# Performance work log

Hardware: AMD Instinct MI355X
Metric: run time of the kernel (lower is better)

## Reference

```python
import jax, jax.numpy as jnp
import numpy as np

B, T, C, H = 16, 512, 256, 8
HS_T = C // H   # temporal head size = 32
HS_S = T // H   # spatial head size = 64
EPS = 1e-6


def _ln(x, w, b):
    m = x.mean(-1, keepdims=True)
    v = ((x - m) ** 2).mean(-1, keepdims=True)
    return (x - m) / jnp.sqrt(v + EPS) * w + b


def setup_inputs() -> dict:
    key = jax.random.key(0)
    ks = jax.random.split(key, 16)
    rn = lambda k, s, scale: jax.random.normal(k, s, dtype=jnp.float32) * scale
    inp = {
        "x_T": rn(ks[0], (B, T, C), 1.0),
        "x_S": rn(ks[1], (B, C, T), 1.0),
        # temporal attention: per-head q/k/v projections, stacked [H, hs, C]
        "Wq_t": rn(ks[2], (H, HS_T, C), C ** -0.5),
        "Wk_t": rn(ks[3], (H, HS_T, C), C ** -0.5),
        "Wv_t": rn(ks[4], (H, HS_T, C), C ** -0.5),
        "Wo": rn(ks[5], (C, C), C ** -0.5),
        # spatial attention: per-head q/k over the time axis, stacked [H, hs_s, T]
        "Wq_s": rn(ks[6], (H, HS_S, T), T ** -0.5),
        "Wk_s": rn(ks[7], (H, HS_S, T), T ** -0.5),
        # feed-forward blocks (expansion_factor=4)
        "ff1_w1": rn(ks[8], (4 * C, C), C ** -0.5),
        "ff1_b1": jnp.zeros((4 * C,), jnp.float32),
        "ff1_w2": rn(ks[9], (C, 4 * C), (4 * C) ** -0.5),
        "ff1_b2": jnp.zeros((C,), jnp.float32),
        "ff2_w1": rn(ks[10], (4 * C, C), C ** -0.5),
        "ff2_b1": jnp.zeros((4 * C,), jnp.float32),
        "ff2_w2": rn(ks[11], (C, 4 * C), (4 * C) ** -0.5),
        "ff2_b2": jnp.zeros((C,), jnp.float32),
        # layernorm affine params
        "t_ln1_w": jnp.ones((C,), jnp.float32), "t_ln1_b": jnp.zeros((C,), jnp.float32),
        "t_ln2_w": jnp.ones((C,), jnp.float32), "t_ln2_b": jnp.zeros((C,), jnp.float32),
        "s_ln1_w": jnp.ones((T,), jnp.float32), "s_ln1_b": jnp.zeros((T,), jnp.float32),
        "fus_ln_w": jnp.ones((C,), jnp.float32), "fus_ln_b": jnp.zeros((C,), jnp.float32),
    }
    return inp


def reference(x_T, x_S, Wq_t, Wk_t, Wv_t, Wo, Wq_s, Wk_s,
              ff1_w1, ff1_b1, ff1_w2, ff1_b2, ff2_w1, ff2_b1, ff2_w2, ff2_b2,
              t_ln1_w, t_ln1_b, t_ln2_w, t_ln2_b, s_ln1_w, s_ln1_b,
              fus_ln_w, fus_ln_b):
    # ---- temporal (causal) multi-head attention ----
    h = _ln(x_T, t_ln1_w, t_ln1_b)                         # [B,T,C]
    q = jnp.einsum('btc,hdc->bhtd', h, Wq_t)
    k = jnp.einsum('btc,hdc->bhtd', h, Wk_t)
    v = jnp.einsum('btc,hdc->bhtd', h, Wv_t)
    scores = jnp.einsum('bhtd,bhsd->bhts', q, k) / jnp.sqrt(jnp.float32(HS_T))
    causal = jnp.tril(jnp.ones((T, T), dtype=bool))
    scores = jnp.where(causal, scores, -jnp.inf)
    att = jax.nn.softmax(scores, axis=-1)
    o = jnp.einsum('bhts,bhsd->bhtd', att, v)              # [B,H,T,hs]
    o = o.transpose(0, 2, 1, 3).reshape(B, T, C)           # concat heads
    attn_out = o @ Wo.T
    x = x_T + attn_out
    # FFN 1
    h2 = _ln(x, t_ln2_w, t_ln2_b)
    f = jax.nn.relu(h2 @ ff1_w1.T + ff1_b1) @ ff1_w2.T + ff1_b2
    temporal_out = x + f                                   # [B,T,C]
    # ---- spatial (non-causal) attention over neurons ----
    hs = _ln(x_S, s_ln1_w, s_ln1_b)                        # [B,C,T]
    qs = jnp.einsum('bct,hdt->bhcd', hs, Wq_s)
    ks = jnp.einsum('bct,hdt->bhcd', hs, Wk_s)
    sc = jnp.einsum('bhcd,bhed->bhce', qs, ks) / jnp.sqrt(jnp.float32(HS_S))
    spatial_weights = jax.nn.softmax(sc, axis=-1).mean(axis=1)   # [B,C,C], mean over heads
    # ---- fusion ----
    fused = jnp.einsum('bce,bte->btc', spatial_weights, temporal_out)
    x2 = temporal_out + fused
    h3 = _ln(x2, fus_ln_w, fus_ln_b)
    f2 = jax.nn.relu(h3 @ ff2_w1.T + ff2_b1) @ ff2_w2.T + ff2_b2
    out = x2 + f2
    return out, spatial_weights
```

## Files before the change

### kernel.cpp

```cpp
#include <hip/hip_runtime.h>
#include <hip/hip_bf16.h>

typedef __hip_bfloat16 bf16;
typedef __attribute__((ext_vector_type(8))) short short8;
typedef __attribute__((ext_vector_type(4))) float f32x4;

#define F_BIAS 1
#define F_RELU 2
#define F_RES  4

__device__ __forceinline__ void st_out(float* p, float v){ *p = v; }
__device__ __forceinline__ void st_out(bf16* p, float v){ *p = __float2bfloat16(v); }
__device__ __forceinline__ short f2bs(float f){
  bf16 h = __float2bfloat16(f);
  return *reinterpret_cast<short*>(&h);
}

__device__ __forceinline__ void gl_lds16(const void* g, void* l){
  __builtin_amdgcn_global_load_lds(
      (const __attribute__((address_space(1))) void*)g,
      (__attribute__((address_space(3))) void*)l, 16, 0, 0);
}

__device__ __forceinline__ void lgkm_barrier(){
  asm volatile("s_waitcnt lgkmcnt(0)" ::: "memory");
  __builtin_amdgcn_s_barrier();
}

struct ProArgs {
  const float* wsrc[10];
  bf16* wdst[10];
  const float *xT, *xS, *tl1w, *tl1b, *sl1w, *sl1b;
  bf16 *hT, *hS;
};

template<int RL>
__device__ __forceinline__ void wave_ln(bf16* __restrict__ dst,
    const float* __restrict__ src, const float* __restrict__ w,
    const float* __restrict__ bvec, int row){
  int lane = threadIdx.x & 63;
  const float* s = src + (size_t)row*RL;
  float4 v0 = *(const float4*)(s + lane*4);
  float4 v1 = {0.f,0.f,0.f,0.f};
  float sum = v0.x+v0.y+v0.z+v0.w;
  float sq  = v0.x*v0.x+v0.y*v0.y+v0.z*v0.z+v0.w*v0.w;
  if (RL == 512){
    v1 = *(const float4*)(s + 256 + lane*4);
    sum += v1.x+v1.y+v1.z+v1.w;
    sq  += v1.x*v1.x+v1.y*v1.y+v1.z*v1.z+v1.w*v1.w;
  }
  #pragma unroll
  for (int off=32; off; off>>=1){
    sum += __shfl_xor(sum, off, 64);
    sq  += __shfl_xor(sq , off, 64);
  }
  const float inv = 1.0f/(float)RL;
  float mean = sum*inv;
  float rstd = rsqrtf(sq*inv - mean*mean + 1e-6f);
  float4 w0 = *(const float4*)(w + lane*4);
  float4 b0 = *(const float4*)(bvec + lane*4);
  bf16* d = dst + (size_t)row*RL;
  short4 o;
  o.x = f2bs((v0.x-mean)*rstd*w0.x + b0.x);
  o.y = f2bs((v0.y-mean)*rstd*w0.y + b0.y);
  o.z = f2bs((v0.z-mean)*rstd*w0.z + b0.z);
  o.w = f2bs((v0.w-mean)*rstd*w0.w + b0.w);
  *(short4*)((short*)d + lane*4) = o;
  if (RL == 512){
    float4 w1 = *(const float4*)(w + 256 + lane*4);
    float4 b1 = *(const float4*)(bvec + 256 + lane*4);
    short4 o1;
    o1.x = f2bs((v1.x-mean)*rstd*w1.x + b1.x);
    o1.y = f2bs((v1.y-mean)*rstd*w1.y + b1.y);
    o1.z = f2bs((v1.z-mean)*rstd*w1.z + b1.z);
    o1.w = f2bs((v1.w-mean)*rstd*w1.w + b1.w);
    *(short4*)((short*)d + 256 + lane*4) = o1;
  }
}

__global__ __launch_bounds__(256) void prologue(ProArgs a){
  int blk = blockIdx.x;
  int wid = threadIdx.x >> 6;
  if (blk < 1792){
    int v = blk*256 + threadIdx.x;
    int e = v*4;
    int seg = (e>=65536)+(e>=131072)+(e>=196608)+(e>=262144)+(e>=524288)
            + (e>=786432)+(e>=1048576)+(e>=1310720)+(e>=1572864);
    const int starts[10] = {0,65536,131072,196608,262144,524288,786432,
                            1048576,1310720,1572864};
    int off = e - starts[seg];
    float4 f = *(const float4*)(a.wsrc[seg] + off);
    short4 o;
    o.x = f2bs(f.x); o.y = f2bs(f.y); o.z = f2bs(f.z); o.w = f2bs(f.w);
    *(short4*)((short*)a.wdst[seg] + off) = o;
  } else if (blk < 1792 + 2048){
    wave_ln<256>(a.hT, a.xT, a.tl1w, a.tl1b, (blk-1792)*4 + wid);
  } else {
    wave_ln<512>(a.hS, a.xS, a.sl1w, a.sl1b, (blk-3840)*4 + wid);
  }
}

template<int BM, int BN, int BK>
__device__ __forceinline__ void gemm_body(
    short* __restrict__ AsB, short* __restrict__ BsB,
    const bf16* __restrict__ A, const bf16* __restrict__ B,
    float* __restrict__ outF, bf16* __restrict__ outB,
    const float* __restrict__ bias, const float* __restrict__ resid,
    int K, int lda, int ldb, int ldc, int flags, int m0, int n0){
  int tid = threadIdx.x;
  int w = tid>>6, lane = tid&63, quad = lane>>4, l16 = lane&15;
  constexpr int MF  = BM/32;
  constexpr int NF  = BN/32;
  constexpr int CPR = BK/8;
  constexpr int CA  = BM*CPR/256;
  constexpr int CB  = BN*CPR/256;
  int wm = (w>>1)*(BM/2), wn = (w&1)*(BN/2);
  f32x4 acc[MF][NF];
  #pragma unroll
  for (int r=0;r<MF;r++)
    #pragma unroll
    for (int j=0;j<NF;j++)
      acc[r][j] = (f32x4){0.f,0.f,0.f,0.f};

  auto stage = [&](int k0, int half){
    short* as = AsB + half*(BM*BK);
    short* bs = BsB + half*(BN*BK);
    #pragma unroll
    for (int c=0;c<CA;c++){
      int ch = tid + c*256;
      int row = ch / CPR, p = ch % CPR;
      gl_lds16(A + (size_t)(m0+row)*lda + k0 + ((p ^ (row&(CPR-1)))*8),
               &as[row*BK + p*8]);
    }
    #pragma unroll
    for (int c=0;c<CB;c++){
      int ch = tid + c*256;
      int row = ch / CPR, p = ch % CPR;
      gl_lds16(B + (size_t)(n0+row)*ldb + k0 + ((p ^ (row&(CPR-1)))*8),
               &bs[row*BK + p*8]);
    }
  };

  stage(0, 0);
  int nk = K / BK;
  for (int t = 0; t < nk; ++t){
    __syncthreads();
    if (t+1 < nk) stage((t+1)*BK, (t+1)&1);
    const short* as = AsB + (t&1)*(BM*BK);
    const short* bs = BsB + (t&1)*(BN*BK);
    #pragma unroll
    for (int ks=0; ks<BK/32; ++ks){
      short8 af[MF], bfr[NF];
      #pragma unroll
      for (int r=0;r<MF;r++){
        int rr = wm + r*16 + l16;
        af[r] = *(short8*)&as[rr*BK + (((ks*4+quad) ^ (rr&(CPR-1)))*8)];
      }
      #pragma unroll
      for (int j=0;j<NF;j++){
        int rr = wn + j*16 + l16;
        bfr[j] = *(short8*)&bs[rr*BK + (((ks*4+quad) ^ (rr&(CPR-1)))*8)];
      }
      #pragma unroll
      for (int r=0;r<MF;r++)
        #pragma unroll
        for (int j=0;j<NF;j++)
          acc[r][j] = __builtin_amdgcn_mfma_f32_16x16x32_bf16(af[r], bfr[j], acc[r][j], 0,0,0);
    }
  }
  #pragma unroll
  for (int r=0;r<MF;r++){
    int mb = m0 + wm + r*16 + quad*4;
    #pragma unroll
    for (int j=0;j<NF;j++){
      int n = n0 + wn + j*16 + l16;
      float bv = (flags & F_BIAS) ? bias[n] : 0.0f;
      #pragma unroll
      for (int e=0;e<4;e++){
        float v = acc[r][j][e] + bv;
        if (flags & F_RELU) v = fmaxf(v, 0.0f);
        long long idx = (long long)(mb+e)*ldc + n;
        if (flags & F_RES) v += resid[idx];
        if (outF) outF[idx] = v;
        if (outB) st_out(outB + idx, v);
      }
    }
  }
}

struct GArgs {
  const bf16 *A, *B;
  float* outF; bf16* outB;
  const float *bias, *resid;
  int K, lda, ldb, ldc, flags, ty;
};
__global__ __launch_bounds__(256) void gemm_dual(GArgs g0, GArgs g1, int n0){
  __shared__ __align__(16) short As[2*128*64];
  __shared__ __align__(16) short Bs[2*128*64];
  int id = blockIdx.x;
  bool first = id < n0;
  const GArgs& g = first ? g0 : g1;
  int t = first ? id : id - n0;
  int bx = t / g.ty, by = t - bx*g.ty;
  gemm_body<128,128,64>(As, Bs, g.A, g.B, g.outF, g.outB, g.bias, g.resid,
                        g.K, g.lda, g.ldb, g.ldc, g.flags, bx*128, by*128);
}

struct LnFfnArgs {
  const bf16 *A;
  const bf16 *Bm;
  const float *resid0;
  const float *lnw, *lnb;
  const bf16 *W1; const float *B1;
  const bf16 *W2; const float *B2;
  float *outF; bf16 *outB;
  long long sA, sB, sR, sO;
};

__global__ __launch_bounds__(512) void lnffn(LnFfnArgs a){
  __shared__ __align__(16) short Hin[32*256];
  __shared__ __align__(16) short Hs[32*1024];
  float (*redS)[32] = (float(*)[32])Hs;
  float (*redQ)[32] = (float(*)[32])(Hs + 512);
  int bz = blockIdx.z;
  const bf16* A  = a.A  + (size_t)bz*a.sA;
  const bf16* Bm = a.Bm + (size_t)bz*a.sB;
  long long rbase = (long long)bz*a.sR;
  long long obase = (long long)bz*a.sO;
  int tid = threadIdx.x;
  int w = tid>>6, lane = tid&63, quad = lane>>4, l16 = lane&15;
  int m0 = blockIdx.x*32;

  f32x4 acc0[2][2];
  #pragma unroll
  for (int r=0;r<2;r++)
    #pragma unroll
    for (int j=0;j<2;j++) acc0[r][j] = (f32x4){0.f,0.f,0.f,0.f};
  #pragma unroll
  for (int ks=0; ks<8; ++ks){
    short8 af[2], bk[2];
    #pragma unroll
    for (int r=0;r<2;r++)
      af[r] = *(const short8*)(A + (size_t)(m0 + r*16 + l16)*256 + ks*32 + quad*8);
    #pragma unroll
    for (int j=0;j<2;j++)
      bk[j] = *(const short8*)(Bm + (size_t)(w*32 + j*16 + l16)*256 + ks*32 + quad*8);
    #pragma unroll
    for (int r=0;r<2;r++)
      #pragma unroll
      for (int j=0;j<2;j++)
        acc0[r][j] = __builtin_amdgcn_mfma_f32_16x16x32_bf16(af[r], bk[j], acc0[r][j], 0,0,0);
  }
  #pragma unroll
  for (int r=0;r<2;r++)
    #pragma unroll
    for (int e=0;e<4;e++){
      int row = r*16 + quad*4 + e;
      float s = 0.f, q2 = 0.f;
      #pragma unroll
      for (int j=0;j<2;j++){
        float v = acc0[r][j][e] +
                  a.resid0[rbase + (long long)(m0+row)*256 + w*32 + j*16 + l16];
        acc0[r][j][e] = v;
        s += v; q2 += v*v;
      }
      #pragma unroll
      for (int off=1; off<16; off<<=1){
        s  += __shfl_xor(s , off, 16);
        q2 += __shfl_xor(q2, off, 16);
      }
      if (l16==0){ redS[w][row] = s; redQ[w][row] = q2; }
    }
  __syncthreads();
  #pragma unroll
  for (int r=0;r<2;r++)
    #pragma unroll
    for (int e=0;e<4;e++){
      int row = r*16 + quad*4 + e;
      float tot = 0.f, tq = 0.f;
      #pragma unroll
      for (int ww=0; ww<8; ww++){ tot += redS[ww][row]; tq += redQ[ww][row]; }
      float mean = tot * (1.0f/256.0f);
      float var  = tq * (1.0f/256.0f) - mean*mean;
      float rstd = rsqrtf(var + 1e-6f);
      #pragma unroll
      for (int j=0;j<2;j++){
        int col = w*32 + j*16 + l16;
        float h = (acc0[r][j][e]-mean)*rstd*a.lnw[col] + a.lnb[col];
        int g = col >> 3;
        Hin[row*256 + ((g ^ row)*8) + (col&7)] = f2bs(h);
      }
    }
  __syncthreads();

  for (int hc=0; hc<2; ++hc){
    f32x4 acc1[2][4];
    #pragma unroll
    for (int r=0;r<2;r++)
      #pragma unroll
      for (int j=0;j<4;j++) acc1[r][j] = (f32x4){0.f,0.f,0.f,0.f};
    #pragma unroll
    for (int ks=0; ks<8; ++ks){
      short8 af[2], bk[4];
      #pragma unroll
      for (int r=0;r<2;r++){
        int rr = r*16 + l16;
        int kk = ks*4 + quad;
        af[r] = *(short8*)&Hin[rr*256 + ((kk ^ rr)*8)];
      }
      #pragma unroll
      for (int j=0;j<4;j++){
        int hr = w*128 + hc*64 + j*16 + l16;
        bk[j] = *(const short8*)(a.W1 + (size_t)hr*256 + ks*32 + quad*8);
      }
      #pragma unroll
      for (int r=0;r<2;r++)
        #pragma unroll
        for (int j=0;j<4;j++)
          acc1[r][j] = __builtin_amdgcn_mfma_f32_16x16x32_bf16(af[r], bk[j], acc1[r][j], 0,0,0);
    }
    #pragma unroll
    for (int r=0;r<2;r++)
      #pragma unroll
      for (int j=0;j<4;j++)
        #pragma unroll
        for (int e=0;e<4;e++){
          int row = r*16 + quad*4 + e;
          int col = w*128 + hc*64 + j*16 + l16;
          float v = fmaxf(acc1[r][j][e] + a.B1[col], 0.0f);
          int g = col>>3;
          Hs[row*1024 + ((g ^ (row&7))*8) + (col&7)] = f2bs(v);
        }
  }
  __syncthreads();

  f32x4 accB[2][2];
  #pragma unroll
  for (int r=0;r<2;r++)
    #pragma unroll
    for (int j=0;j<2;j++) accB[r][j] = (f32x4){0.f,0.f,0.f,0.f};
  #pragma unroll 8
  for (int ks=0; ks<32; ++ks){
    short8 af[2], bk[2];
    #pragma unroll
    for (int r=0;r<2;r++){
      int rr = r*16 + l16;
      int kk = ks*4 + quad;
      af[r] = *(short8*)&Hs[rr*1024 + ((kk ^ (rr&7))*8)];
    }
    #pragma unroll
    for (int j=0;j<2;j++){
      int n = w*32 + j*16 + l16;
      bk[j] = *(const short8*)(a.W2 + (size_t)n*1024 + ks*32 + quad*8);
    }
    #pragma unroll
    for (int r=0;r<2;r++)
      #pragma unroll
      for (int j=0;j<2;j++)
        accB[r][j] = __builtin_amdgcn_mfma_f32_16x16x32_bf16(af[r], bk[j], accB[r][j], 0,0,0);
  }
  #pragma unroll
  for (int r=0;r<2;r++)
    #pragma unroll
    for (int j=0;j<2;j++){
      int n = w*32 + j*16 + l16;
      float bv = a.B2[n];
      #pragma unroll
      for (int e=0;e<4;e++){
        int row = r*16 + quad*4 + e;
        long long idx = obase + (long long)(m0+row)*256 + n;
        float v = accB[r][j][e] + bv + acc0[r][j][e];
        a.outF[idx] = v;
        if (a.outB) st_out(a.outB + idx, v);
      }
    }
}

__device__ __forceinline__ int fsw(int row){ return (row>>1)&3; }
__global__ __launch_bounds__(256) void flash_mfma(
    const bf16* __restrict__ qkv, bf16* __restrict__ o){
  int qt = (int)gridDim.x - 1 - (int)blockIdx.x;
  int h = blockIdx.y, b = blockIdx.z;
  int tid = threadIdx.x;
  int w = tid>>6, lane = tid&63, quad = lane>>4, l16 = lane&15;
  __shared__ __align__(16) bf16 Qs[64*32];
  __shared__ __align__(16) bf16 Ks[2][64*32];
  __shared__ __align__(16) bf16 Vt[2][32*72];
  __shared__ __align__(16) bf16 Ps[64*72];
  const bf16* base = qkv + (size_t)b*512*768;
  int t0 = qt*64;
  int srow = tid>>2, spos = tid&3;
  gl_lds16(base + (size_t)(t0+srow)*768 + h*32 + ((spos ^ fsw(srow))*8),
           &Qs[srow*32 + spos*8]);
  {
    const bf16* rp = base + (size_t)srow*768 + h*32;
    gl_lds16(rp + 256 + ((spos ^ fsw(srow))*8), &Ks[0][srow*32 + spos*8]);
    short8 v = *(const short8*)(rp + 512 + spos*8);
    #pragma unroll
    for (int q=0;q<8;q++){
      short tmp = v[q];
      Vt[0][(spos*8+q)*72 + srow] = *(bf16*)&tmp;
    }
  }
  f32x4 accO[2];
  accO[0] = (f32x4){0.f,0.f,0.f,0.f};
  accO[1] = (f32x4){0.f,0.f,0.f,0.f};
  float m_i[4], l_i[4];
  #pragma unroll
  for (int e=0;e<4;e++){ m_i[e] = -3.0e38f; l_i[e] = 0.0f; }
  const float scale = 0.17677669529663687f;
  __syncthreads();
  int rq = w*16 + l16;
  short8 aq = *(short8*)&Qs[rq*32 + ((quad ^ fsw(rq))*8)];

  for (int kt = 0; kt <= qt; ++kt){
    if (kt) __syncthreads();
    int cur = kt&1, nxt = cur^1;
    bool pre = (kt < qt);
    short8 vpre;
    if (pre){
      const bf16* rp = base + (size_t)((kt+1)*64 + srow)*768 + h*32;
      gl_lds16(rp + 256 + ((spos ^ fsw(srow))*8), &Ks[nxt][srow*32 + spos*8]);
      vpre = *(const short8*)(rp + 512 + spos*8);
    }
    f32x4 S[4];
    #pragma unroll
    for (int j2=0;j2<4;j2++){
      int rk = j2*16 + l16;
      short8 bk = *(short8*)&Ks[cur][rk*32 + ((quad ^ fsw(rk))*8)];
      S[j2] = __builtin_amdgcn_mfma_f32_16x16x32_bf16(aq, bk,
                (f32x4){0.f,0.f,0.f,0.f}, 0,0,0);
    }
    bool diag = (kt == qt);
    int s0 = kt*64;
    int qrow_base = t0 + w*16 + quad*4;
    #pragma unroll
    for (int e=0;e<4;e++){
      float sv[4];
      #pragma unroll
      for (int j2=0;j2<4;j2++){
        float x = S[j2][e]*scale;
        if (diag && (s0 + j2*16 + l16 > qrow_base + e)) x = -3.0e38f;
        sv[j2] = x;
      }
      float mx = fmaxf(fmaxf(sv[0],sv[1]), fmaxf(sv[2],sv[3]));
      #pragma unroll
      for (int off=1; off<16; off<<=1) mx = fmaxf(mx, __shfl_xor(mx, off, 64));
      float m_new = fmaxf(m_i[e], mx);
      float alpha = __expf(m_i[e]-m_new);
      float rs = 0.0f;
      #pragma unroll
      for (int j2=0;j2<4;j2++){
        float p = __expf(sv[j2]-m_new);
        rs += p;
        Ps[(w*16+quad*4+e)*72 + j2*16 + l16] = __float2bfloat16(p);
      }
      #pragma unroll
      for (int off=1; off<16; off<<=1) rs += __shfl_xor(rs, off, 64);
      l_i[e] = l_i[e]*alpha + rs;
      m_i[e] = m_new;
      accO[0][e] *= alpha;
      accO[1][e] *= alpha;
    }
    asm volatile("s_waitcnt lgkmcnt(0)" ::: "memory");
    __builtin_amdgcn_sched_barrier(0);
    #pragma unroll
    for (int sh=0; sh<2; ++sh){
      short8 ap = *(short8*)&Ps[(w*16+l16)*72 + sh*32 + quad*8];
      #pragma unroll
      for (int dh=0; dh<2; ++dh){
        short8 bv = *(short8*)&Vt[cur][(dh*16+l16)*72 + sh*32 + quad*8];
        accO[dh] = __builtin_amdgcn_mfma_f32_16x16x32_bf16(ap, bv, accO[dh], 0,0,0);
      }
    }
    if (pre){
      #pragma unroll
      for (int q=0;q<8;q++){
        short tmp = vpre[q];
        Vt[nxt][(spos*8+q)*72 + srow] = *(bf16*)&tmp;
      }
    }
  }
  #pragma unroll
  for (int e=0;e<4;e++){
    float inv = 1.0f/l_i[e];
    int t = t0 + w*16 + quad*4 + e;
    bf16* op = o + ((size_t)(b*512+t))*256 + h*32 + l16;
    op[0]  = __float2bfloat16(accO[0][e]*inv);
    op[16] = __float2bfloat16(accO[1][e]*inv);
  }
}

__global__ __launch_bounds__(256) void spatial_fused(
    const bf16* __restrict__ qk, float* __restrict__ out1,
    bf16* __restrict__ swB){
  int ct = blockIdx.x & 15, b = blockIdx.x >> 4;
  int tid = threadIdx.x;
  int w = tid>>6, lane = tid&63, quad = lane>>4, l16 = lane&15;
  __shared__ __align__(16) bf16 Qall[16*512];
  __shared__ __align__(16) bf16 Ks[2][256*64];
  __shared__ float redM[4][16], redS2[4][16];
  const bf16* qbase = qk + ((size_t)(b*256 + ct*16))*1024;
  #pragma unroll
  for (int c=0;c<4;c++){
    int ch = tid + c*256;
    int row = ch>>6, p = ch&63;
    gl_lds16(qbase + (size_t)row*1024 + ((p ^ (row&7))*8), &Qall[row*512 + p*8]);
  }
  auto stageK = [&](int h, int half){
    bf16* ks = Ks[half];
    #pragma unroll
    for (int c=0;c<8;c++){
      int ch = tid + c*256;
      int e = ch>>3, p = ch&7;
      gl_lds16(qk + ((size_t)(b*256 + e))*1024 + 512 + h*64 + ((p ^ (e&7))*8),
               &ks[e*64 + p*8]);
    }
  };
  stageK(0, 0);
  float fRes[4][4];
  #pragma unroll
  for (int j=0;j<4;j++)
    #pragma unroll
    for (int e=0;e<4;e++) fRes[j][e] = 0.0f;

  for (int h=0; h<8; ++h){
    __syncthreads();
    if (h+1 < 8) stageK(h+1, (h+1)&1);
    const bf16* kcur = Ks[h&1];
    f32x4 acc[4];
    #pragma unroll
    for (int j=0;j<4;j++) acc[j] = (f32x4){0.f,0.f,0.f,0.f};
    #pragma unroll
    for (int ki=0; ki<2; ++ki){
      int g = h*8 + ki*4 + quad;
      short8 aq = *(short8*)&Qall[l16*512 + ((g ^ (l16&7))*8)];
      #pragma unroll
      for (int j=0;j<4;j++){
        int e = w*64 + j*16 + l16;
        short8 bk = *(short8*)&kcur[e*64 + (((ki*4+quad) ^ (e&7))*8)];
        acc[j] = __builtin_amdgcn_mfma_f32_16x16x32_bf16(aq, bk, acc[j], 0,0,0);
      }
    }
    #pragma unroll
    for (int e=0;e<4;e++){
      float m = -3.0e38f;
      #pragma unroll
      for (int j=0;j<4;j++){
        float s = acc[j][e]*0.125f;
        acc[j][e] = s;
        m = fmaxf(m, s);
      }
      #pragma unroll
      for (int off=1; off<16; off<<=1) m = fmaxf(m, __shfl_xor(m, off, 16));
      if (l16==0) redM[w][quad*4+e] = m;
    }
    lgkm_barrier();
    #pragma unroll
    for (int e=0;e<4;e++){
      int r = quad*4+e;
      float m = fmaxf(fmaxf(redM[0][r],redM[1][r]), fmaxf(redM[2][r],redM[3][r]));
      float s = 0.0f;
      #pragma unroll
      for (int j=0;j<4;j++){
        float p = __expf(acc[j][e]-m);
        acc[j][e] = p; s += p;
      }
      #pragma unroll
      for (int off=1; off<16; off<<=1) s += __shfl_xor(s, off, 16);
      if (l16==0) redS2[w][r] = s;
    }
    lgkm_barrier();
    #pragma unroll
    for (int e=0;e<4;e++){
      int r = quad*4+e;
      float tot = redS2[0][r]+redS2[1][r]+redS2[2][r]+redS2[3][r];
      float inv = 0.125f/tot;
      #pragma unroll
      for (int j=0;j<4;j++) fRes[j][e] += acc[j][e]*inv;
    }
  }
  #pragma unroll
  for (int e=0;e<4;e++){
    int c = ct*16 + quad*4 + e;
    size_t rb = ((size_t)b*256 + c)*256;
    #pragma unroll
    for (int j=0;j<4;j++){
      int col = w*64 + j*16 + l16;
      out1[rb+col] = fRes[j][e];
      swB[rb+col]  = __float2bfloat16(fRes[j][e]);
    }
  }
}

extern "C" void kernel_launch(void* const* d_in, const int* in_sizes, int n_in,
                              void* d_out, int out_size, void* d_ws, size_t ws_size,
                              hipStream_t stream){
  (void)in_sizes; (void)n_in; (void)out_size; (void)ws_size;
  const float* x_T  = (const float*)d_in[0];
  const float* x_S  = (const float*)d_in[1];
  const float* Wq_t = (const float*)d_in[2];
  const float* Wk_t = (const float*)d_in[3];
  const float* Wv_t = (const float*)d_in[4];
  const float* Wo   = (const float*)d_in[5];
  const float* Wq_s = (const float*)d_in[6];
  const float* Wk_s = (const float*)d_in[7];
  const float* f1w1 = (const float*)d_in[8];
  const float* f1b1 = (const float*)d_in[9];
  const float* f1w2 = (const float*)d_in[10];
  const float* f1b2 = (const float*)d_in[11];
  const float* f2w1 = (const float*)d_in[12];
  const float* f2b1 = (const float*)d_in[13];
  const float* f2w2 = (const float*)d_in[14];
  const float* f2b2 = (const float*)d_in[15];
  const float* tl1w = (const float*)d_in[16];
  const float* tl1b = (const float*)d_in[17];
  const float* tl2w = (const float*)d_in[18];
  const float* tl2b = (const float*)d_in[19];
  const float* sl1w = (const float*)d_in[20];
  const float* sl1b = (const float*)d_in[21];
  const float* flw  = (const float*)d_in[22];
  const float* flb  = (const float*)d_in[23];

  float* ws = (float*)d_ws;
  size_t off = 0;
  bf16*  Wqkvb  = (bf16*)(ws + off); off += 768*256/2;
  bf16*  Wob    = (bf16*)(ws + off); off += 256*256/2;
  bf16*  f1w1b  = (bf16*)(ws + off); off += 1024*256/2;
  bf16*  f1w2b  = (bf16*)(ws + off); off += 256*1024/2;
  bf16*  f2w1b  = (bf16*)(ws + off); off += 1024*256/2;
  bf16*  f2w2b  = (bf16*)(ws + off); off += 256*1024/2;
  bf16*  WSb    = (bf16*)(ws + off); off += 1024*512/2;
  bf16*  bufHb  = (bf16*)(ws + off); off += (size_t)8192*256/2;
  bf16*  bufHSb = (bf16*)(ws + off); off += (size_t)4096*512/2;
  bf16*  bufQKVb= (bf16*)(ws + off); off += (size_t)8192*768/2;
  bf16*  bufOb  = (bf16*)(ws + off); off += (size_t)8192*256/2;
  bf16*  bufTOb = (bf16*)(ws + off); off += (size_t)8192*256/2;
  bf16*  swB    = (bf16*)(ws + off); off += (size_t)16*256*256/2;
  bf16*  qkB    = (bf16*)(ws + off); off += (size_t)4096*1024/2;
  float* bufTO  = ws + off; off += (size_t)8192*256;

  float* out0 = (float*)d_out;
  float* out1 = out0 + (size_t)16*512*256;

  ProArgs pa;
  pa.wsrc[0]=Wq_t;  pa.wdst[0]=Wqkvb;
  pa.wsrc[1]=Wk_t;  pa.wdst[1]=Wqkvb+65536;
  pa.wsrc[2]=Wv_t;  pa.wdst[2]=Wqkvb+131072;
  pa.wsrc[3]=Wo;    pa.wdst[3]=Wob;
  pa.wsrc[4]=f1w1;  pa.wdst[4]=f1w1b;
  pa.wsrc[5]=f1w2;  pa.wdst[5]=f1w2b;
  pa.wsrc[6]=f2w1;  pa.wdst[6]=f2w1b;
  pa.wsrc[7]=f2w2;  pa.wdst[7]=f2w2b;
  pa.wsrc[8]=Wq_s;  pa.wdst[8]=WSb;
  pa.wsrc[9]=Wk_s;  pa.wdst[9]=WSb+262144;
  pa.xT=x_T; pa.xS=x_S; pa.tl1w=tl1w; pa.tl1b=tl1b;
  pa.sl1w=sl1w; pa.sl1b=sl1b; pa.hT=bufHb; pa.hS=bufHSb;
  prologue<<<4864,256,0,stream>>>(pa);

  GArgs gq, gs;
  gq.A=bufHb;  gq.B=Wqkvb; gq.outF=nullptr; gq.outB=bufQKVb;
  gq.bias=nullptr; gq.resid=nullptr;
  gq.K=256; gq.lda=256; gq.ldb=256; gq.ldc=768; gq.flags=0; gq.ty=6;
  gs.A=bufHSb; gs.B=WSb;   gs.outF=nullptr; gs.outB=qkB;
  gs.bias=nullptr; gs.resid=nullptr;
  gs.K=512; gs.lda=512; gs.ldb=512; gs.ldc=1024; gs.flags=0; gs.ty=8;
  gemm_dual<<<640,256,0,stream>>>(gq, gs, 384);

  spatial_fused<<<256,256,0,stream>>>(qkB, out1, swB);

  flash_mfma<<<dim3(8,8,16),256,0,stream>>>(bufQKVb, bufOb);

  LnFfnArgs la1;
  la1.A=bufOb; la1.Bm=Wob; la1.resid0=x_T; la1.lnw=tl2w; la1.lnb=tl2b;
  la1.W1=f1w1b; la1.B1=f1b1; la1.W2=f1w2b; la1.B2=f1b2;
  la1.outF=bufTO; la1.outB=bufTOb;
  la1.sA=0; la1.sB=0; la1.sR=0; la1.sO=0;
  lnffn<<<dim3(256,1,1),512,0,stream>>>(la1);

  LnFfnArgs la2;
  la2.A=bufTOb; la2.Bm=swB; la2.resid0=bufTO; la2.lnw=flw; la2.lnb=flb;
  la2.W1=f2w1b; la2.B1=f2b1; la2.W2=f2w2b; la2.B2=f2b2;
  la2.outF=out0; la2.outB=nullptr;
  la2.sA=131072; la2.sB=65536; la2.sR=131072; la2.sO=131072;
  lnffn<<<dim3(16,1,16),512,0,stream>>>(la2);
}
```

Measured before the change: 284.9 us.

## Split lnffn row tiles across 16 waves with 1024-thread blocks

The fused LN+FFN kernel now launches 1024 threads per block instead of 512. Waves are arranged as a 2x8 grid, so each wave handles one 16-row slab instead of two. This halves per-wave accumulator registers and doubles the waves available to hide latency. In exchange, every weight fragment (W1, W2, Bm) is now read by twice as many waves from global memory, which raises cache and bandwidth traffic.

```diff
diff --git a/kernel.cpp b/kernel.cpp
--- a/kernel.cpp
+++ b/kernel.cpp
@@ -217,7 +217,7 @@
   long long sA, sB, sR, sO;
 };
 
-__global__ __launch_bounds__(512) void lnffn(LnFfnArgs a){
+__global__ __launch_bounds__(1024) void lnffn(LnFfnArgs a){
   __shared__ __align__(16) short Hin[32*256];
   __shared__ __align__(16) short Hs[32*1024];
   float (*redS)[32] = (float(*)[32])Hs;
@@ -230,150 +230,116 @@
   int tid = threadIdx.x;
   int w = tid>>6, lane = tid&63, quad = lane>>4, l16 = lane&15;
   int m0 = blockIdx.x*32;
-
-  f32x4 acc0[2][2];
-  #pragma unroll
-  for (int r=0;r<2;r++)
-    #pragma unroll
-    for (int j=0;j<2;j++) acc0[r][j] = (f32x4){0.f,0.f,0.f,0.f};
+  int wm = (w>>3)*16;
+  int wc = (w&7);
+
+  f32x4 acc0[2];
+  acc0[0] = (f32x4){0.f,0.f,0.f,0.f};
+  acc0[1] = (f32x4){0.f,0.f,0.f,0.f};
   #pragma unroll
   for (int ks=0; ks<8; ++ks){
-    short8 af[2], bk[2];
-    #pragma unroll
-    for (int r=0;r<2;r++)
-      af[r] = *(const short8*)(A + (size_t)(m0 + r*16 + l16)*256 + ks*32 + quad*8);
-    #pragma unroll
-    for (int j=0;j<2;j++)
-      bk[j] = *(const short8*)(Bm + (size_t)(w*32 + j*16 + l16)*256 + ks*32 + quad*8);
-    #pragma unroll
-    for (int r=0;r<2;r++)
-      #pragma unroll
-      for (int j=0;j<2;j++)
-        acc0[r][j] = __builtin_amdgcn_mfma_f32_16x16x32_bf16(af[r], bk[j], acc0[r][j], 0,0,0);
-  }
-  #pragma unroll
-  for (int r=0;r<2;r++)
-    #pragma unroll
-    for (int e=0;e<4;e++){
-      int row = r*16 + quad*4 + e;
-      float s = 0.f, q2 = 0.f;
-      #pragma unroll
-      for (int j=0;j<2;j++){
-        float v = acc0[r][j][e] +
-                  a.resid0[rbase + (long long)(m0+row)*256 + w*32 + j*16 + l16];
-        acc0[r][j][e] = v;
-        s += v; q2 += v*v;
-      }
-      #pragma unroll
-      for (int off=1; off<16; off<<=1){
-        s  += __shfl_xor(s , off, 16);
-        q2 += __shfl_xor(q2, off, 16);
-      }
-      if (l16==0){ redS[w][row] = s; redQ[w][row] = q2; }
-    }
+    short8 af = *(const short8*)(A + (size_t)(m0 + wm + l16)*256 + ks*32 + quad*8);
+    #pragma unroll
+    for (int j=0;j<2;j++){
+      short8 bk = *(const short8*)(Bm + (size_t)(wc*32 + j*16 + l16)*256 + ks*32 + quad*8);
+      acc0[j] = __builtin_amdgcn_mfma_f32_16x16x32_bf16(af, bk, acc0[j], 0,0,0);
+    }
+  }
+  #pragma unroll
+  for (int e=0;e<4;e++){
+    int row = wm + quad*4 + e;
+    float s = 0.f, q2 = 0.f;
+    #pragma unroll
+    for (int j=0;j<2;j++){
+      float v = acc0[j][e] +
+                a.resid0[rbase + (long long)(m0+row)*256 + wc*32 + j*16 + l16];
+      acc0[j][e] = v;
+      s += v; q2 += v*v;
+    }
+    #pragma unroll
+    for (int off=1; off<16; off<<=1){
+      s  += __shfl_xor(s , off, 16);
+      q2 += __shfl_xor(q2, off, 16);
+    }
+    if (l16==0){ redS[wc][row] = s; redQ[wc][row] = q2; }
+  }
   __syncthreads();
   #pragma unroll
-  for (int r=0;r<2;r++)
-    #pragma unroll
-    for (int e=0;e<4;e++){
-      int row = r*16 + quad*4 + e;
-      float tot = 0.f, tq = 0.f;
-      #pragma unroll
-      for (int ww=0; ww<8; ww++){ tot += redS[ww][row]; tq += redQ[ww][row]; }
-      float mean = tot * (1.0f/256.0f);
-      float var  = tq * (1.0f/256.0f) - mean*mean;
-      float rstd = rsqrtf(var + 1e-6f);
-      #pragma unroll
-      for (int j=0;j<2;j++){
-        int col = w*32 + j*16 + l16;
-        float h = (acc0[r][j][e]-mean)*rstd*a.lnw[col] + a.lnb[col];
-        int g = col >> 3;
-        Hin[row*256 + ((g ^ row)*8) + (col&7)] = f2bs(h);
-      }
-    }
+  for (int e=0;e<4;e++){
+    int row = wm + quad*4 + e;
+    float tot = 0.f, tq = 0.f;
+    #pragma unroll
+    for (int ww=0; ww<8; ww++){ tot += redS[ww][row]; tq += redQ[ww][row]; }
+    float mean = tot * (1.0f/256.0f);
+    float var  = tq * (1.0f/256.0f) - mean*mean;
+    float rstd = rsqrtf(var + 1e-6f);
+    #pragma unroll
+    for (int j=0;j<2;j++){
+      int col = wc*32 + j*16 + l16;
+      float h = (acc0[j][e]-mean)*rstd*a.lnw[col] + a.lnb[col];
+      int g = col >> 3;
+      Hin[row*256 + ((g ^ row)*8) + (col&7)] = f2bs(h);
+    }
+  }
   __syncthreads();
 
   for (int hc=0; hc<2; ++hc){
-    f32x4 acc1[2][4];
-    #pragma unroll
-    for (int r=0;r<2;r++)
-      #pragma unroll
-      for (int j=0;j<4;j++) acc1[r][j] = (f32x4){0.f,0.f,0.f,0.f};
+    f32x4 acc1[4];
+    #pragma unroll
+    for (int j=0;j<4;j++) acc1[j] = (f32x4){0.f,0.f,0.f,0.f};
     #pragma unroll
     for (int ks=0; ks<8; ++ks){
-      short8 af[2], bk[4];
-      #pragma unroll
-      for (int r=0;r<2;r++){
-        int rr = r*16 + l16;
-        int kk = ks*4 + quad;
-        af[r] = *(short8*)&Hin[rr*256 + ((kk ^ rr)*8)];
-      }
+      int rr = wm + l16;
+      int kk = ks*4 + quad;
+      short8 af = *(short8*)&Hin[rr*256 + ((kk ^ rr)*8)];
       #pragma unroll
       for (int j=0;j<4;j++){
-        int hr = w*128 + hc*64 + j*16 + l16;
-        bk[j] = *(const short8*)(a.W1 + (size_t)hr*256 + ks*32 + quad*8);
-      }
-      #pragma unroll
-      for (int r=0;r<2;r++)
-        #pragma unroll
-        for (int j=0;j<4;j++)
-          acc1[r][j] = __builtin_amdgcn_mfma_f32_16x16x32_bf16(af[r], bk[j], acc1[r][j], 0,0,0);
-    }
-    #pragma unroll
-    for (int r=0;r<2;r++)
-      #pragma unroll
-      for (int j=0;j<4;j++)
-        #pragma unroll
-        for (int e=0;e<4;e++){
-          int row = r*16 + quad*4 + e;
-          int col = w*128 + hc*64 + j*16 + l16;
-          float v = fmaxf(acc1[r][j][e] + a.B1[col], 0.0f);
-          int g = col>>3;
-          Hs[row*1024 + ((g ^ (row&7))*8) + (col&7)] = f2bs(v);
-        }
+        int hr = wc*128 + hc*64 + j*16 + l16;
+        short8 bk = *(const short8*)(a.W1 + (size_t)hr*256 + ks*32 + quad*8);
+        acc1[j] = __builtin_amdgcn_mfma_f32_16x16x32_bf16(af, bk, acc1[j], 0,0,0);
+      }
+    }
+    #pragma unroll
+    for (int j=0;j<4;j++)
+      #pragma unroll
+      for (int e=0;e<4;e++){
+        int row = wm + quad*4 + e;
+        int col = wc*128 + hc*64 + j*16 + l16;
+        float v = fmaxf(acc1[j][e] + a.B1[col], 0.0f);
+        int g = col>>3;
+        Hs[row*1024 + ((g ^ (row&7))*8) + (col&7)] = f2bs(v);
+      }
   }
   __syncthreads();
 
-  f32x4 accB[2][2];
-  #pragma unroll
-  for (int r=0;r<2;r++)
-    #pragma unroll
-    for (int j=0;j<2;j++) accB[r][j] = (f32x4){0.f,0.f,0.f,0.f};
+  f32x4 accB[2];
+  accB[0] = (f32x4){0.f,0.f,0.f,0.f};
+  accB[1] = (f32x4){0.f,0.f,0.f,0.f};
   #pragma unroll 8
   for (int ks=0; ks<32; ++ks){
-    short8 af[2], bk[2];
-    #pragma unroll
-    for (int r=0;r<2;r++){
-      int rr = r*16 + l16;
-      int kk = ks*4 + quad;
-      af[r] = *(short8*)&Hs[rr*1024 + ((kk ^ (rr&7))*8)];
-    }
+    int rr = wm + l16;
+    int kk = ks*4 + quad;
+    short8 af = *(short8*)&Hs[rr*1024 + ((kk ^ (rr&7))*8)];
     #pragma unroll
     for (int j=0;j<2;j++){
-      int n = w*32 + j*16 + l16;
-      bk[j] = *(const short8*)(a.W2 + (size_t)n*1024 + ks*32 + quad*8);
-    }
-    #pragma unroll
-    for (int r=0;r<2;r++)
-      #pragma unroll
-      for (int j=0;j<2;j++)
-        accB[r][j] = __builtin_amdgcn_mfma_f32_16x16x32_bf16(af[r], bk[j], accB[r][j], 0,0,0);
-  }
-  #pragma unroll
-  for (int r=0;r<2;r++)
-    #pragma unroll
-    for (int j=0;j<2;j++){
-      int n = w*32 + j*16 + l16;
-      float bv = a.B2[n];
-      #pragma unroll
-      for (int e=0;e<4;e++){
-        int row = r*16 + quad*4 + e;
-        long long idx = obase + (long long)(m0+row)*256 + n;
-        float v = accB[r][j][e] + bv + acc0[r][j][e];
-        a.outF[idx] = v;
-        if (a.outB) st_out(a.outB + idx, v);
-      }
-    }
+      int n = wc*32 + j*16 + l16;
+      short8 bk = *(const short8*)(a.W2 + (size_t)n*1024 + ks*32 + quad*8);
+      accB[j] = __builtin_amdgcn_mfma_f32_16x16x32_bf16(af, bk, accB[j], 0,0,0);
+    }
+  }
+  #pragma unroll
+  for (int j=0;j<2;j++){
+    int n = wc*32 + j*16 + l16;
+    float bv = a.B2[n];
+    #pragma unroll
+    for (int e=0;e<4;e++){
+      int row = wm + quad*4 + e;
+      long long idx = obase + (long long)(m0+row)*256 + n;
+      float v = accB[j][e] + bv + acc0[j][e];
+      a.outF[idx] = v;
+      if (a.outB) st_out(a.outB + idx, v);
+    }
+  }
 }
 
 __device__ __forceinline__ int fsw(int row){ return (row>>1)&3; }
@@ -676,12 +642,12 @@
   la1.W1=f1w1b; la1.B1=f1b1; la1.W2=f1w2b; la1.B2=f1b2;
   la1.outF=bufTO; la1.outB=bufTOb;
   la1.sA=0; la1.sB=0; la1.sR=0; la1.sO=0;
-  lnffn<<<dim3(256,1,1),512,0,stream>>>(la1);
+  lnffn<<<dim3(256,1,1),1024,0,stream>>>(la1);
 
   LnFfnArgs la2;
   la2.A=bufTOb; la2.Bm=swB; la2.resid0=bufTO; la2.lnw=flw; la2.lnb=flb;
   la2.W1=f2w1b; la2.B1=f2b1; la2.W2=f2w2b; la2.B2=f2b2;
   la2.outF=out0; la2.outB=nullptr;
   la2.sA=131072; la2.sB=65536; la2.sR=131072; la2.sO=131072;
-  lnffn<<<dim3(16,1,16),512,0,stream>>>(la2);
-}
+  lnffn<<<dim3(16,1,16),1024,0,stream>>>(la2);
+}
```

Result: slower. 341.7 us (+20.0%).
